# Kernel tuning notes

Measured on AMD Instinct MI355X. Metric: run time of the kernel, lower is better.

Reference implementation:

```python
import jax, jax.numpy as jnp
import numpy as np

N, E, R, D = 100000, 300000, 2, 128


def setup_inputs() -> dict:
    key = jax.random.key(0)
    k0, k1, k2, k3, k4 = jax.random.split(key, 5)
    x = jax.random.normal(k0, (N, D), dtype=jnp.float32)
    attn_w = jax.random.normal(k1, (R, 2 * D), dtype=jnp.float32) / np.sqrt(2 * D).astype(np.float32)
    loop_weight = jax.random.normal(k2, (D, D), dtype=jnp.float32) / np.sqrt(D).astype(np.float32)
    h_bias = jnp.zeros((D,), dtype=jnp.float32)
    src = jax.random.randint(k3, (R, E), 0, N, dtype=jnp.int32)
    dst = jax.random.randint(k4, (R, E), 0, N, dtype=jnp.int32)
    return {"x": x, "attn_w": attn_w, "loop_weight": loop_weight, "h_bias": h_bias,
            "src": src, "dst": dst}


def _rel_attention(x, a, src_r, dst_r):
    # Per-edge score: attn_fc(cat(src feat, dst feat)) with Linear(2D -> 1, no bias).
    d = x.shape[1]
    xs = x[src_r]                     # [E, D] gathered source features (the messages m)
    e = xs @ a[:d] + x[dst_r] @ a[d:]  # [E] edge logits (note: no leaky_relu in message_fc path)
    # Segment (per-destination mailbox) softmax, numerically stable.
    m = jax.ops.segment_max(e, dst_r, num_segments=N)
    p = jnp.exp(e - m[dst_r])
    denom = jax.ops.segment_sum(p, dst_r, num_segments=N)
    alpha = p / jnp.maximum(denom[dst_r], jnp.float32(1e-30))  # [E]
    # Weighted scatter-sum of messages back to destination nodes.
    return jax.ops.segment_sum(alpha[:, None] * xs, dst_r, num_segments=N)  # [N, D]


def reference(x, attn_w, loop_weight, h_bias, src, dst):
    # multi_update_all(..., 'sum'): sum the per-relation attention aggregations.
    agg = _rel_attention(x, attn_w[0], src[0], dst[0])
    for r in range(1, R):
        agg = agg + _rel_attention(x, attn_w[r], src[r], dst[r])
    # self loop + bias (activation=None, dropout=0)
    h = agg + x @ loop_weight + h_bias
    return h
```

## Files before the change

kernel.cpp:

```cpp
#include <hip/hip_runtime.h>

#define N_NODES 100000
#define N_EDGES 300000
#define DIM     128
#define NBINS   (2 * N_NODES)
#define CNT_STRIDE 8
#define SLOT_CAP 24
#define WCONV_BLOCKS 8
#define BIN_BLOCKS  ((N_EDGES + 255) / 256)
#define SCORE_BLOCKS (N_NODES / 4)
#define ZERO_BLOCKS ((NBINS * CNT_STRIDE / 4 + 255) / 256)
#define FUSE_BLOCKS (N_NODES / 16)

typedef __attribute__((ext_vector_type(8))) short bfrag;
typedef __attribute__((ext_vector_type(4))) float f32x4;

__device__ __forceinline__ unsigned short f2bf(float f) {
  unsigned int u = __float_as_uint(f);
  u += 0x7FFFu + ((u >> 16) & 1u);
  return (unsigned short)(u >> 16);
}
__device__ __forceinline__ float bflo(unsigned int u) { return __uint_as_float(u << 16); }
__device__ __forceinline__ float bfhi(unsigned int u) { return __uint_as_float(u & 0xffff0000u); }

__global__ __launch_bounds__(256) void k0_zero_kernel(int* __restrict__ counts) {
  int i = blockIdx.x * 256 + threadIdx.x;
  if (i < NBINS * CNT_STRIDE / 4) ((int4*)counts)[i] = make_int4(0, 0, 0, 0);
}

__global__ __launch_bounds__(256) void k1_bin_scores_kernel(
    const float* __restrict__ x, const float* __restrict__ attn_w,
    const float* __restrict__ W,
    const int* __restrict__ src, const int* __restrict__ dst,
    float* __restrict__ pexp, int* __restrict__ counts, int* __restrict__ slots,
    unsigned short* __restrict__ Wt, unsigned short* __restrict__ x_bf) {
  if (blockIdx.x < WCONV_BLOCKS) {
    for (int e = blockIdx.x * 256 + threadIdx.x; e < DIM * DIM; e += WCONV_BLOCKS * 256) {
      int k = e >> 7, c = e & 127;
      Wt[c * DIM + k] = f2bf(W[e]);
    }
    return;
  }
  if (blockIdx.x < WCONV_BLOCKS + BIN_BLOCKS) {
    int idx = (blockIdx.x - WCONV_BLOCKS) * 256 + threadIdx.x;
    if (idx < N_EDGES) {
      int d0 = dst[idx];
      int d1 = dst[idx + N_EDGES];
      int s0 = src[idx];
      int s1 = src[idx + N_EDGES];
      int p0 = atomicAdd(&counts[(size_t)(d0 * 2 + 0) * CNT_STRIDE], 1);
      int p1 = atomicAdd(&counts[(size_t)(d1 * 2 + 1) * CNT_STRIDE], 1);
      if (p0 < SLOT_CAP)
        __builtin_nontemporal_store(s0, &slots[(size_t)(d0 * 2 + 0) * SLOT_CAP + p0]);
      if (p1 < SLOT_CAP)
        __builtin_nontemporal_store(s1, &slots[(size_t)(d1 * 2 + 1) * SLOT_CAP + p1]);
    }
    return;
  }
  int wave = (((blockIdx.x - WCONV_BLOCKS - BIN_BLOCKS) * 256) + threadIdx.x) >> 6;
  int lane = threadIdx.x & 63;
  if (wave >= N_NODES) return;
  float2 a0 = ((const float2*)(attn_w +   0))[lane];
  float2 a1 = ((const float2*)(attn_w + 256))[lane];
  float2 v = ((const float2*)(x + (size_t)wave * DIM))[lane];
  ushort2 bv; bv.x = f2bf(v.x); bv.y = f2bf(v.y);
  ((ushort2*)(x_bf + (size_t)wave * DIM))[lane] = bv;
  float p0 = v.x * a0.x + v.y * a0.y;
  float p1 = v.x * a1.x + v.y * a1.y;
  #pragma unroll
  for (int off = 32; off > 0; off >>= 1) {
    p0 += __shfl_down(p0, off, 64);
    p1 += __shfl_down(p1, off, 64);
  }
  if (lane == 0) {
    pexp[wave]           = __expf(p0);
    pexp[N_NODES + wave] = __expf(p1);
  }
}

__global__ __launch_bounds__(256) void k2_gemm_agg_kernel(
    const int* __restrict__ slots, const int* __restrict__ counts,
    const float* __restrict__ pexp,
    const unsigned short* __restrict__ x_bf, const unsigned short* __restrict__ Wt,
    const float* __restrict__ bias, float* __restrict__ out) {
  __shared__ float gtile[16][DIM];
  int r0 = blockIdx.x * 16;
  int w  = threadIdx.x >> 6;
  int wl = threadIdx.x & 63;
  {
    int n = wl & 15, q = wl >> 4;
    const unsigned short* xrow = x_bf + (size_t)(r0 + n) * DIM;
    f32x4 acc[2];
    #pragma unroll
    for (int c = 0; c < 2; c++) {
      float bv = bias[(2 * w + c) * 16 + n];
      acc[c] = (f32x4){bv, bv, bv, bv};
    }
    #pragma unroll
    for (int kc = 0; kc < 4; kc++) {
      int k0 = kc * 32 + q * 8;
      bfrag a = *((const bfrag*)(xrow + k0));
      #pragma unroll
      for (int c = 0; c < 2; c++) {
        bfrag b = *((const bfrag*)(Wt + (size_t)((2 * w + c) * 16 + n) * DIM + k0));
        acc[c] = __builtin_amdgcn_mfma_f32_16x16x32_bf16(a, b, acc[c], 0, 0, 0);
      }
    }
    #pragma unroll
    for (int c = 0; c < 2; c++) {
      #pragma unroll
      for (int rr = 0; rr < 4; rr++) {
        gtile[q * 4 + rr][(2 * w + c) * 16 + n] = acc[c][rr];
      }
    }
  }
  __syncthreads();
  int rrel = wl >> 5;
  int l    = wl & 31;
  int nbase = r0 + w * 4;
  int cnt[4]; int sj[4]; float pj[4]; float dinv[4];
  #pragma unroll
  for (int nn = 0; nn < 4; nn++) {
    int c = counts[(size_t)((nbase + nn) * 2 + rrel) * CNT_STRIDE];
    cnt[nn] = (c > SLOT_CAP) ? SLOT_CAP : c;
  }
  #pragma unroll
  for (int nn = 0; nn < 4; nn++) {
    sj[nn] = 0;
    if (l < cnt[nn]) sj[nn] = slots[(size_t)((nbase + nn) * 2 + rrel) * SLOT_CAP + l];
  }
  #pragma unroll
  for (int nn = 0; nn < 4; nn++) {
    pj[nn] = (l < cnt[nn]) ? pexp[rrel * N_NODES + sj[nn]] : 0.f;
  }
  #pragma unroll
  for (int nn = 0; nn < 4; nn++) {
    float d = pj[nn];
    #pragma unroll
    for (int off = 16; off > 0; off >>= 1) d += __shfl_xor(d, off, 64);
    dinv[nn] = (cnt[nn] > 0) ? 1.f / d : 0.f;
  }
  #pragma unroll
  for (int nn = 0; nn < 4; nn++) {
    int node = nbase + nn;
    float4 accr = make_float4(0.f, 0.f, 0.f, 0.f);
    int cn = cnt[nn];
    int j = 0;
    for (; j + 4 <= cn; j += 4) {
      int   s0 = __shfl(sj[nn], j + 0, 32); float q0 = __shfl(pj[nn], j + 0, 32);
      int   s1 = __shfl(sj[nn], j + 1, 32); float q1 = __shfl(pj[nn], j + 1, 32);
      int   s2 = __shfl(sj[nn], j + 2, 32); float q2 = __shfl(pj[nn], j + 2, 32);
      int   s3 = __shfl(sj[nn], j + 3, 32); float q3 = __shfl(pj[nn], j + 3, 32);
      uint2 g0 = ((const uint2*)(x_bf + (size_t)s0 * DIM))[l];
      uint2 g1 = ((const uint2*)(x_bf + (size_t)s1 * DIM))[l];
      uint2 g2 = ((const uint2*)(x_bf + (size_t)s2 * DIM))[l];
      uint2 g3 = ((const uint2*)(x_bf + (size_t)s3 * DIM))[l];
      accr.x += q0*bflo(g0.x) + q1*bflo(g1.x) + q2*bflo(g2.x) + q3*bflo(g3.x);
      accr.y += q0*bfhi(g0.x) + q1*bfhi(g1.x) + q2*bfhi(g2.x) + q3*bfhi(g3.x);
      accr.z += q0*bflo(g0.y) + q1*bflo(g1.y) + q2*bflo(g2.y) + q3*bflo(g3.y);
      accr.w += q0*bfhi(g0.y) + q1*bfhi(g1.y) + q2*bfhi(g2.y) + q3*bfhi(g3.y);
    }
    for (; j < cn; j++) {
      int   s0 = __shfl(sj[nn], j, 32); float q0 = __shfl(pj[nn], j, 32);
      uint2 g0 = ((const uint2*)(x_bf + (size_t)s0 * DIM))[l];
      accr.x += q0*bflo(g0.x); accr.y += q0*bfhi(g0.x);
      accr.z += q0*bflo(g0.y); accr.w += q0*bfhi(g0.y);
    }
    float4 agg;
    agg.x = accr.x * dinv[nn];
    agg.y = accr.y * dinv[nn];
    agg.z = accr.z * dinv[nn];
    agg.w = accr.w * dinv[nn];
    agg.x += __shfl_xor(agg.x, 32, 64);
    agg.y += __shfl_xor(agg.y, 32, 64);
    agg.z += __shfl_xor(agg.z, 32, 64);
    agg.w += __shfl_xor(agg.w, 32, 64);
    if (wl < 32) {
      const float4 g = *((const float4*)&gtile[w * 4 + nn][4 * wl]);
      float4 o;
      o.x = g.x + agg.x;
      o.y = g.y + agg.y;
      o.z = g.z + agg.z;
      o.w = g.w + agg.w;
      ((float4*)(out + (size_t)node * DIM))[wl] = o;
    }
  }
}

extern "C" void kernel_launch(void* const* d_in, const int* in_sizes, int n_in,
                              void* d_out, int out_size, void* d_ws, size_t ws_size,
                              hipStream_t stream) {
  const float* x      = (const float*)d_in[0];
  const float* attn_w = (const float*)d_in[1];
  const float* loop_w = (const float*)d_in[2];
  const float* h_bias = (const float*)d_in[3];
  const int*   src    = (const int*)d_in[4];
  const int*   dst    = (const int*)d_in[5];
  float*       out    = (float*)d_out;

  float*          pexp   = (float*)d_ws;
  int*            counts = (int*)(pexp + NBINS);
  int*            slots  = counts + (size_t)NBINS * CNT_STRIDE;
  unsigned short* Wt     = (unsigned short*)(slots + (size_t)NBINS * SLOT_CAP);
  unsigned short* x_bf   = Wt + DIM * DIM;

  k0_zero_kernel<<<ZERO_BLOCKS, 256, 0, stream>>>(counts);
  k1_bin_scores_kernel<<<WCONV_BLOCKS + BIN_BLOCKS + SCORE_BLOCKS, 256, 0, stream>>>(
      x, attn_w, loop_w, src, dst, pexp, counts, slots, Wt, x_bf);
  k2_gemm_agg_kernel<<<FUSE_BLOCKS, 256, 0, stream>>>(
      slots, counts, pexp, x_bf, Wt, h_bias, out);
}
```

Baseline: 227.7 us.

## Merge three kernels into one persistent cooperative kernel with grid syncs

Replaces the zero/bin/score/GEMM-aggregate kernel sequence with a single cooperative persistent kernel that uses grid-wide syncs between phases. The bf16 transposed weight is built straight into swizzled LDS per block instead of global memory. Scores are now computed 16 lanes per row, and the neighbor gather is unrolled so up to six row loads per node are issued up front. The aim is to remove launch gaps and boost memory-level parallelism, at the cost of two grid barriers, lower occupancy from the 32KB LDS, and a fallback three-kernel path when cooperative launch is unavailable.

```diff
diff --git a/kernel.cpp b/kernel.cpp
--- a/kernel.cpp
+++ b/kernel.cpp
@@ -1,4 +1,7 @@
 #include <hip/hip_runtime.h>
+#include <hip/hip_cooperative_groups.h>
+
+namespace cg = cooperative_groups;
 
 #define N_NODES 100000
 #define N_EDGES 300000
@@ -6,14 +9,13 @@
 #define NBINS   (2 * N_NODES)
 #define CNT_STRIDE 8
 #define SLOT_CAP 24
-#define WCONV_BLOCKS 8
-#define BIN_BLOCKS  ((N_EDGES + 255) / 256)
-#define SCORE_BLOCKS (N_NODES / 4)
-#define ZERO_BLOCKS ((NBINS * CNT_STRIDE / 4 + 255) / 256)
-#define FUSE_BLOCKS (N_NODES / 16)
+#define ROW_TILES (N_NODES / 16)
+#define UNR 6
 
 typedef __attribute__((ext_vector_type(8))) short bfrag;
 typedef __attribute__((ext_vector_type(4))) float f32x4;
+typedef __attribute__((ext_vector_type(4))) unsigned short u16x4;
+typedef __attribute__((ext_vector_type(2))) unsigned int   u32x2;
 
 __device__ __forceinline__ unsigned short f2bf(float f) {
   unsigned int u = __float_as_uint(f);
@@ -23,70 +25,82 @@
 __device__ __forceinline__ float bflo(unsigned int u) { return __uint_as_float(u << 16); }
 __device__ __forceinline__ float bfhi(unsigned int u) { return __uint_as_float(u & 0xffff0000u); }
 
-__global__ __launch_bounds__(256) void k0_zero_kernel(int* __restrict__ counts) {
-  int i = blockIdx.x * 256 + threadIdx.x;
-  if (i < NBINS * CNT_STRIDE / 4) ((int4*)counts)[i] = make_int4(0, 0, 0, 0);
-}
-
-__global__ __launch_bounds__(256) void k1_bin_scores_kernel(
-    const float* __restrict__ x, const float* __restrict__ attn_w,
-    const float* __restrict__ W,
-    const int* __restrict__ src, const int* __restrict__ dst,
-    float* __restrict__ pexp, int* __restrict__ counts, int* __restrict__ slots,
-    unsigned short* __restrict__ Wt, unsigned short* __restrict__ x_bf) {
-  if (blockIdx.x < WCONV_BLOCKS) {
-    for (int e = blockIdx.x * 256 + threadIdx.x; e < DIM * DIM; e += WCONV_BLOCKS * 256) {
-      int k = e >> 7, c = e & 127;
-      Wt[c * DIM + k] = f2bf(W[e]);
-    }
-    return;
-  }
-  if (blockIdx.x < WCONV_BLOCKS + BIN_BLOCKS) {
-    int idx = (blockIdx.x - WCONV_BLOCKS) * 256 + threadIdx.x;
-    if (idx < N_EDGES) {
-      int d0 = dst[idx];
-      int d1 = dst[idx + N_EDGES];
-      int s0 = src[idx];
-      int s1 = src[idx + N_EDGES];
-      int p0 = atomicAdd(&counts[(size_t)(d0 * 2 + 0) * CNT_STRIDE], 1);
-      int p1 = atomicAdd(&counts[(size_t)(d1 * 2 + 1) * CNT_STRIDE], 1);
-      if (p0 < SLOT_CAP)
-        __builtin_nontemporal_store(s0, &slots[(size_t)(d0 * 2 + 0) * SLOT_CAP + p0]);
-      if (p1 < SLOT_CAP)
-        __builtin_nontemporal_store(s1, &slots[(size_t)(d1 * 2 + 1) * SLOT_CAP + p1]);
-    }
-    return;
-  }
-  int wave = (((blockIdx.x - WCONV_BLOCKS - BIN_BLOCKS) * 256) + threadIdx.x) >> 6;
-  int lane = threadIdx.x & 63;
-  if (wave >= N_NODES) return;
-  float2 a0 = ((const float2*)(attn_w +   0))[lane];
-  float2 a1 = ((const float2*)(attn_w + 256))[lane];
-  float2 v = ((const float2*)(x + (size_t)wave * DIM))[lane];
-  ushort2 bv; bv.x = f2bf(v.x); bv.y = f2bf(v.y);
-  ((ushort2*)(x_bf + (size_t)wave * DIM))[lane] = bv;
-  float p0 = v.x * a0.x + v.y * a0.y;
-  float p1 = v.x * a1.x + v.y * a1.y;
-  #pragma unroll
-  for (int off = 32; off > 0; off >>= 1) {
-    p0 += __shfl_down(p0, off, 64);
-    p1 += __shfl_down(p1, off, 64);
-  }
-  if (lane == 0) {
-    pexp[wave]           = __expf(p0);
-    pexp[N_NODES + wave] = __expf(p1);
-  }
-}
-
-__global__ __launch_bounds__(256) void k2_gemm_agg_kernel(
+__device__ __forceinline__ void do_zero(int* counts, int start, int stride) {
+  for (int i = start; i < NBINS * CNT_STRIDE / 4; i += stride)
+    ((int4*)counts)[i] = make_int4(0, 0, 0, 0);
+}
+
+__device__ __forceinline__ void do_wt_lds(unsigned short* WtS, const float* W, int tid) {
+  for (int e = tid; e < DIM * DIM; e += 256) {
+    int k = e >> 7, c = e & 127;
+    int byte = c * 256 + k * 2;
+    int swz = byte ^ ((c & 7) << 4);
+    WtS[swz >> 1] = f2bf(W[e]);
+  }
+}
+
+__device__ __forceinline__ void do_bin(const int* __restrict__ src,
+                                       const int* __restrict__ dst,
+                                       int* __restrict__ counts, int* __restrict__ slots,
+                                       int start, int stride) {
+  for (int e = start; e < N_EDGES; e += stride) {
+    int d0 = __builtin_nontemporal_load(&dst[e]);
+    int d1 = __builtin_nontemporal_load(&dst[e + N_EDGES]);
+    int s0 = __builtin_nontemporal_load(&src[e]);
+    int s1 = __builtin_nontemporal_load(&src[e + N_EDGES]);
+    int p0 = atomicAdd(&counts[(size_t)(d0 * 2 + 0) * CNT_STRIDE], 1);
+    int p1 = atomicAdd(&counts[(size_t)(d1 * 2 + 1) * CNT_STRIDE], 1);
+    if (p0 < SLOT_CAP)
+      __builtin_nontemporal_store(s0, &slots[(size_t)(d0 * 2 + 0) * SLOT_CAP + p0]);
+    if (p1 < SLOT_CAP)
+      __builtin_nontemporal_store(s1, &slots[(size_t)(d1 * 2 + 1) * SLOT_CAP + p1]);
+  }
+}
+
+__device__ __forceinline__ void do_scores(const float* __restrict__ x,
+                                          const float* __restrict__ attn_w,
+                                          float* __restrict__ pexp,
+                                          unsigned short* __restrict__ x_bf,
+                                          int tid, int bstart, int bstride) {
+  int t    = tid & 15;
+  int rsub = tid >> 4;
+  const f32x4* A0 = (const f32x4*)attn_w;
+  const f32x4* A1 = (const f32x4*)(attn_w + 2 * DIM);
+  f32x4 a00 = A0[t], a01 = A0[t + 16];
+  f32x4 a10 = A1[t], a11 = A1[t + 16];
+  for (int tb = bstart; tb < ROW_TILES; tb += bstride) {
+    int row = tb * 16 + rsub;
+    const f32x4* xr = (const f32x4*)(x + (size_t)row * DIM);
+    f32x4 v0 = __builtin_nontemporal_load(xr + t);
+    f32x4 v1 = __builtin_nontemporal_load(xr + t + 16);
+    u16x4 b0, b1;
+    b0.x = f2bf(v0.x); b0.y = f2bf(v0.y); b0.z = f2bf(v0.z); b0.w = f2bf(v0.w);
+    b1.x = f2bf(v1.x); b1.y = f2bf(v1.y); b1.z = f2bf(v1.z); b1.w = f2bf(v1.w);
+    u16x4* xb = (u16x4*)(x_bf + (size_t)row * DIM);
+    xb[t] = b0; xb[t + 16] = b1;
+    float p0 = v0.x*a00.x + v0.y*a00.y + v0.z*a00.z + v0.w*a00.w
+             + v1.x*a01.x + v1.y*a01.y + v1.z*a01.z + v1.w*a01.w;
+    float p1 = v0.x*a10.x + v0.y*a10.y + v0.z*a10.z + v0.w*a10.w
+             + v1.x*a11.x + v1.y*a11.y + v1.z*a11.z + v1.w*a11.w;
+    #pragma unroll
+    for (int off = 8; off > 0; off >>= 1) {
+      p0 += __shfl_xor(p0, off, 64);
+      p1 += __shfl_xor(p1, off, 64);
+    }
+    if (t == 0) {
+      pexp[row]           = __expf(p0);
+      pexp[N_NODES + row] = __expf(p1);
+    }
+  }
+}
+
+__device__ __forceinline__ void do_tile(const unsigned short* WtS, float (*gtile)[DIM],
     const int* __restrict__ slots, const int* __restrict__ counts,
-    const float* __restrict__ pexp,
-    const unsigned short* __restrict__ x_bf, const unsigned short* __restrict__ Wt,
-    const float* __restrict__ bias, float* __restrict__ out) {
-  __shared__ float gtile[16][DIM];
-  int r0 = blockIdx.x * 16;
-  int w  = threadIdx.x >> 6;
-  int wl = threadIdx.x & 63;
+    const float* __restrict__ pexp, const unsigned short* __restrict__ x_bf,
+    const float* __restrict__ bias, float* __restrict__ out, int tid, int tb) {
+  int r0 = tb * 16;
+  int w  = tid >> 6;
+  int wl = tid & 63;
   {
     int n = wl & 15, q = wl >> 4;
     const unsigned short* xrow = x_bf + (size_t)(r0 + n) * DIM;
@@ -102,21 +116,21 @@
       bfrag a = *((const bfrag*)(xrow + k0));
       #pragma unroll
       for (int c = 0; c < 2; c++) {
-        bfrag b = *((const bfrag*)(Wt + (size_t)((2 * w + c) * 16 + n) * DIM + k0));
-        acc[c] = __builtin_amdgcn_mfma_f32_16x16x32_bf16(a, b, acc[c], 0, 0, 0);
+        int cc   = (2 * w + c) * 16 + n;
+        int byte = cc * 256 + k0 * 2;
+        const bfrag* bp = (const bfrag*)((const char*)WtS + (byte ^ ((cc & 7) << 4)));
+        acc[c] = __builtin_amdgcn_mfma_f32_16x16x32_bf16(a, *bp, acc[c], 0, 0, 0);
       }
     }
     #pragma unroll
-    for (int c = 0; c < 2; c++) {
+    for (int c = 0; c < 2; c++)
       #pragma unroll
-      for (int rr = 0; rr < 4; rr++) {
+      for (int rr = 0; rr < 4; rr++)
         gtile[q * 4 + rr][(2 * w + c) * 16 + n] = acc[c][rr];
-      }
-    }
   }
   __syncthreads();
-  int rrel = wl >> 5;
-  int l    = wl & 31;
+  int rrel  = wl >> 5;
+  int l     = wl & 31;
   int nbase = r0 + w * 4;
   int cnt[4]; int sj[4]; float pj[4]; float dinv[4];
   #pragma unroll
@@ -125,14 +139,11 @@
     cnt[nn] = (c > SLOT_CAP) ? SLOT_CAP : c;
   }
   #pragma unroll
-  for (int nn = 0; nn < 4; nn++) {
-    sj[nn] = 0;
-    if (l < cnt[nn]) sj[nn] = slots[(size_t)((nbase + nn) * 2 + rrel) * SLOT_CAP + l];
-  }
-  #pragma unroll
-  for (int nn = 0; nn < 4; nn++) {
+  for (int nn = 0; nn < 4; nn++)
+    sj[nn] = (l < cnt[nn]) ? slots[(size_t)((nbase + nn) * 2 + rrel) * SLOT_CAP + l] : 0;
+  #pragma unroll
+  for (int nn = 0; nn < 4; nn++)
     pj[nn] = (l < cnt[nn]) ? pexp[rrel * N_NODES + sj[nn]] : 0.f;
-  }
   #pragma unroll
   for (int nn = 0; nn < 4; nn++) {
     float d = pj[nn];
@@ -140,51 +151,112 @@
     for (int off = 16; off > 0; off >>= 1) d += __shfl_xor(d, off, 64);
     dinv[nn] = (cnt[nn] > 0) ? 1.f / d : 0.f;
   }
-  #pragma unroll
-  for (int nn = 0; nn < 4; nn++) {
-    int node = nbase + nn;
-    float4 accr = make_float4(0.f, 0.f, 0.f, 0.f);
-    int cn = cnt[nn];
-    int j = 0;
-    for (; j + 4 <= cn; j += 4) {
-      int   s0 = __shfl(sj[nn], j + 0, 32); float q0 = __shfl(pj[nn], j + 0, 32);
-      int   s1 = __shfl(sj[nn], j + 1, 32); float q1 = __shfl(pj[nn], j + 1, 32);
-      int   s2 = __shfl(sj[nn], j + 2, 32); float q2 = __shfl(pj[nn], j + 2, 32);
-      int   s3 = __shfl(sj[nn], j + 3, 32); float q3 = __shfl(pj[nn], j + 3, 32);
-      uint2 g0 = ((const uint2*)(x_bf + (size_t)s0 * DIM))[l];
-      uint2 g1 = ((const uint2*)(x_bf + (size_t)s1 * DIM))[l];
-      uint2 g2 = ((const uint2*)(x_bf + (size_t)s2 * DIM))[l];
-      uint2 g3 = ((const uint2*)(x_bf + (size_t)s3 * DIM))[l];
-      accr.x += q0*bflo(g0.x) + q1*bflo(g1.x) + q2*bflo(g2.x) + q3*bflo(g3.x);
-      accr.y += q0*bfhi(g0.x) + q1*bfhi(g1.x) + q2*bfhi(g2.x) + q3*bfhi(g3.x);
-      accr.z += q0*bflo(g0.y) + q1*bflo(g1.y) + q2*bflo(g2.y) + q3*bflo(g3.y);
-      accr.w += q0*bfhi(g0.y) + q1*bfhi(g1.y) + q2*bfhi(g2.y) + q3*bfhi(g3.y);
-    }
-    for (; j < cn; j++) {
-      int   s0 = __shfl(sj[nn], j, 32); float q0 = __shfl(pj[nn], j, 32);
-      uint2 g0 = ((const uint2*)(x_bf + (size_t)s0 * DIM))[l];
-      accr.x += q0*bflo(g0.x); accr.y += q0*bfhi(g0.x);
-      accr.z += q0*bflo(g0.y); accr.w += q0*bfhi(g0.y);
-    }
-    float4 agg;
-    agg.x = accr.x * dinv[nn];
-    agg.y = accr.y * dinv[nn];
-    agg.z = accr.z * dinv[nn];
-    agg.w = accr.w * dinv[nn];
+  u32x2 g[4][UNR];
+  #pragma unroll
+  for (int nn = 0; nn < 4; nn++) {
+    #pragma unroll
+    for (int u = 0; u < UNR; u++) {
+      int s = __shfl(sj[nn], u, 32);
+      if (u < cnt[nn])
+        g[nn][u] = ((const u32x2*)(x_bf + (size_t)s * DIM))[l];
+    }
+  }
+  f32x4 accr[4];
+  #pragma unroll
+  for (int nn = 0; nn < 4; nn++) accr[nn] = (f32x4){0.f, 0.f, 0.f, 0.f};
+  #pragma unroll
+  for (int nn = 0; nn < 4; nn++) {
+    #pragma unroll
+    for (int u = 0; u < UNR; u++) {
+      float qv = __shfl(pj[nn], u, 32);
+      if (u < cnt[nn]) {
+        u32x2 gv = g[nn][u];
+        accr[nn].x += qv * bflo(gv.x);
+        accr[nn].y += qv * bfhi(gv.x);
+        accr[nn].z += qv * bflo(gv.y);
+        accr[nn].w += qv * bfhi(gv.y);
+      }
+    }
+  }
+  #pragma unroll
+  for (int nn = 0; nn < 4; nn++) {
+    for (int j = UNR; j < cnt[nn]; j++) {
+      int   s  = __shfl(sj[nn], j, 32);
+      float qv = __shfl(pj[nn], j, 32);
+      u32x2 gv = ((const u32x2*)(x_bf + (size_t)s * DIM))[l];
+      accr[nn].x += qv * bflo(gv.x); accr[nn].y += qv * bfhi(gv.x);
+      accr[nn].z += qv * bflo(gv.y); accr[nn].w += qv * bfhi(gv.y);
+    }
+  }
+  #pragma unroll
+  for (int nn = 0; nn < 4; nn++) {
+    f32x4 agg;
+    agg.x = accr[nn].x * dinv[nn];
+    agg.y = accr[nn].y * dinv[nn];
+    agg.z = accr[nn].z * dinv[nn];
+    agg.w = accr[nn].w * dinv[nn];
     agg.x += __shfl_xor(agg.x, 32, 64);
     agg.y += __shfl_xor(agg.y, 32, 64);
     agg.z += __shfl_xor(agg.z, 32, 64);
     agg.w += __shfl_xor(agg.w, 32, 64);
     if (wl < 32) {
-      const float4 g = *((const float4*)&gtile[w * 4 + nn][4 * wl]);
-      float4 o;
-      o.x = g.x + agg.x;
-      o.y = g.y + agg.y;
-      o.z = g.z + agg.z;
-      o.w = g.w + agg.w;
-      ((float4*)(out + (size_t)node * DIM))[wl] = o;
-    }
-  }
+      const float* gr = &gtile[w * 4 + nn][4 * wl];
+      f32x4 o;
+      o.x = gr[0] + agg.x; o.y = gr[1] + agg.y;
+      o.z = gr[2] + agg.z; o.w = gr[3] + agg.w;
+      __builtin_nontemporal_store(o, (f32x4*)(out + (size_t)(nbase + nn) * DIM) + wl);
+    }
+  }
+  __syncthreads();
+}
+
+__global__ __launch_bounds__(256, 4) void mega_kernel(
+    const float* __restrict__ x, const float* __restrict__ attn_w,
+    const float* __restrict__ W, const float* __restrict__ bias,
+    const int* __restrict__ src, const int* __restrict__ dst,
+    float* __restrict__ pexp, int* __restrict__ counts, int* __restrict__ slots,
+    unsigned short* __restrict__ x_bf, float* __restrict__ out) {
+  __shared__ unsigned short WtS[DIM * DIM];
+  __shared__ float gtile[16][DIM];
+  int tid  = threadIdx.x;
+  int gtid = blockIdx.x * 256 + tid;
+  int gsz  = gridDim.x * 256;
+  do_wt_lds(WtS, W, tid);
+  do_zero(counts, gtid, gsz);
+  cg::this_grid().sync();
+  do_bin(src, dst, counts, slots, gtid, gsz);
+  do_scores(x, attn_w, pexp, x_bf, tid, blockIdx.x, gridDim.x);
+  cg::this_grid().sync();
+  for (int tb = blockIdx.x; tb < ROW_TILES; tb += gridDim.x)
+    do_tile(WtS, gtile, slots, counts, pexp, x_bf, bias, out, tid, tb);
+}
+
+#define FB_BIN_BLOCKS ((N_EDGES + 255) / 256)
+
+__global__ __launch_bounds__(256) void fb_k0(int* __restrict__ counts) {
+  do_zero(counts, blockIdx.x * 256 + threadIdx.x, gridDim.x * 256);
+}
+__global__ __launch_bounds__(256) void fb_k1(
+    const float* __restrict__ x, const float* __restrict__ attn_w,
+    const int* __restrict__ src, const int* __restrict__ dst,
+    float* __restrict__ pexp, int* __restrict__ counts, int* __restrict__ slots,
+    unsigned short* __restrict__ x_bf) {
+  if (blockIdx.x < FB_BIN_BLOCKS) {
+    do_bin(src, dst, counts, slots, blockIdx.x * 256 + threadIdx.x, FB_BIN_BLOCKS * 256);
+    return;
+  }
+  do_scores(x, attn_w, pexp, x_bf, threadIdx.x, blockIdx.x - FB_BIN_BLOCKS, ROW_TILES);
+}
+__global__ __launch_bounds__(256) void fb_k2(
+    const float* __restrict__ W, const int* __restrict__ slots,
+    const int* __restrict__ counts, const float* __restrict__ pexp,
+    const unsigned short* __restrict__ x_bf, const float* __restrict__ bias,
+    float* __restrict__ out) {
+  __shared__ unsigned short WtS[DIM * DIM];
+  __shared__ float gtile[16][DIM];
+  do_wt_lds(WtS, W, threadIdx.x);
+  __syncthreads();
+  do_tile(WtS, gtile, slots, counts, pexp, x_bf, bias, out, threadIdx.x, blockIdx.x);
 }
 
 extern "C" void kernel_launch(void* const* d_in, const int* in_sizes, int n_in,
@@ -201,12 +273,26 @@
   float*          pexp   = (float*)d_ws;
   int*            counts = (int*)(pexp + NBINS);
   int*            slots  = counts + (size_t)NBINS * CNT_STRIDE;
-  unsigned short* Wt     = (unsigned short*)(slots + (size_t)NBINS * SLOT_CAP);
-  unsigned short* x_bf   = Wt + DIM * DIM;
-
-  k0_zero_kernel<<<ZERO_BLOCKS, 256, 0, stream>>>(counts);
-  k1_bin_scores_kernel<<<WCONV_BLOCKS + BIN_BLOCKS + SCORE_BLOCKS, 256, 0, stream>>>(
-      x, attn_w, loop_w, src, dst, pexp, counts, slots, Wt, x_bf);
-  k2_gemm_agg_kernel<<<FUSE_BLOCKS, 256, 0, stream>>>(
-      slots, counts, pexp, x_bf, Wt, h_bias, out);
-}
+  unsigned short* x_bf   = (unsigned short*)(slots + (size_t)NBINS * SLOT_CAP);
+
+  static int coop_blocks = -2;
+  if (coop_blocks == -2) {
+    int bpc = 0;
+    hipError_t qe = hipOccupancyMaxActiveBlocksPerMultiprocessor(
+        &bpc, (const void*)mega_kernel, 256, 0);
+    coop_blocks = (qe == hipSuccess && bpc >= 1) ? bpc * 256 : -1;
+  }
+  if (coop_blocks > 0) {
+    void* args[] = {(void*)&x, (void*)&attn_w, (void*)&loop_w, (void*)&h_bias,
+                    (void*)&src, (void*)&dst, (void*)&pexp, (void*)&counts,
+                    (void*)&slots, (void*)&x_bf, (void*)&out};
+    hipError_t le = hipLaunchCooperativeKernel((const void*)mega_kernel,
+        dim3(coop_blocks), dim3(256), args, 0, stream);
+    if (le == hipSuccess) return;
+    coop_blocks = -1;
+  }
+  fb_k0<<<(NBINS * CNT_STRIDE / 4 + 255) / 256, 256, 0, stream>>>(counts);
+  fb_k1<<<FB_BIN_BLOCKS + ROW_TILES, 256, 0, stream>>>(
+      x, attn_w, src, dst, pexp, counts, slots, x_bf);
+  fb_k2<<<ROW_TILES, 256, 0, stream>>>(loop_w, slots, counts, pexp, x_bf, h_bias, out);
+}
```

Result: slower. 484.3 us (+112.7%).

## Batch first four neighbor gathers across nodes and use nontemporal memory ops

Applied to the files above, without the earlier changes.

The aggregation kernel now issues the first four neighbor-row gathers for all four nodes of a wave up front, masked by zero weights. Before, it walked each node's edges one node at a time. This raises memory-level parallelism for the typical low-degree mailboxes, at the cost of extra loads for nodes with fewer than four edges. It also loads slot indices unconditionally and pads the shared-memory tile. Edge, feature and output traffic now uses nontemporal loads and stores, and the count-zeroing kernel is replaced with hipMemsetAsync.

```diff
diff --git a/kernel.cpp b/kernel.cpp
--- a/kernel.cpp
+++ b/kernel.cpp
@@ -6,14 +6,17 @@
 #define NBINS   (2 * N_NODES)
 #define CNT_STRIDE 8
 #define SLOT_CAP 24
+#define ROW_TILES (N_NODES / 16)
+#define GDIM (DIM + 4)
+
 #define WCONV_BLOCKS 8
 #define BIN_BLOCKS  ((N_EDGES + 255) / 256)
 #define SCORE_BLOCKS (N_NODES / 4)
-#define ZERO_BLOCKS ((NBINS * CNT_STRIDE / 4 + 255) / 256)
-#define FUSE_BLOCKS (N_NODES / 16)
 
 typedef __attribute__((ext_vector_type(8))) short bfrag;
 typedef __attribute__((ext_vector_type(4))) float f32x4;
+typedef __attribute__((ext_vector_type(2))) float f32x2;
+typedef __attribute__((ext_vector_type(2))) unsigned int   u32x2;
 
 __device__ __forceinline__ unsigned short f2bf(float f) {
   unsigned int u = __float_as_uint(f);
@@ -23,12 +26,7 @@
 __device__ __forceinline__ float bflo(unsigned int u) { return __uint_as_float(u << 16); }
 __device__ __forceinline__ float bfhi(unsigned int u) { return __uint_as_float(u & 0xffff0000u); }
 
-__global__ __launch_bounds__(256) void k0_zero_kernel(int* __restrict__ counts) {
-  int i = blockIdx.x * 256 + threadIdx.x;
-  if (i < NBINS * CNT_STRIDE / 4) ((int4*)counts)[i] = make_int4(0, 0, 0, 0);
-}
-
-__global__ __launch_bounds__(256) void k1_bin_scores_kernel(
+__global__ __launch_bounds__(256) void k1_kernel(
     const float* __restrict__ x, const float* __restrict__ attn_w,
     const float* __restrict__ W,
     const int* __restrict__ src, const int* __restrict__ dst,
@@ -42,12 +40,12 @@
     return;
   }
   if (blockIdx.x < WCONV_BLOCKS + BIN_BLOCKS) {
-    int idx = (blockIdx.x - WCONV_BLOCKS) * 256 + threadIdx.x;
-    if (idx < N_EDGES) {
-      int d0 = dst[idx];
-      int d1 = dst[idx + N_EDGES];
-      int s0 = src[idx];
-      int s1 = src[idx + N_EDGES];
+    int e = (blockIdx.x - WCONV_BLOCKS) * 256 + threadIdx.x;
+    if (e < N_EDGES) {
+      int d0 = __builtin_nontemporal_load(&dst[e]);
+      int d1 = __builtin_nontemporal_load(&dst[e + N_EDGES]);
+      int s0 = __builtin_nontemporal_load(&src[e]);
+      int s1 = __builtin_nontemporal_load(&src[e + N_EDGES]);
       int p0 = atomicAdd(&counts[(size_t)(d0 * 2 + 0) * CNT_STRIDE], 1);
       int p1 = atomicAdd(&counts[(size_t)(d1 * 2 + 1) * CNT_STRIDE], 1);
       if (p0 < SLOT_CAP)
@@ -57,12 +55,12 @@
     }
     return;
   }
-  int wave = (((blockIdx.x - WCONV_BLOCKS - BIN_BLOCKS) * 256) + threadIdx.x) >> 6;
+  int wave = (((blockIdx.x - WCONV_BLOCKS - BIN_BLOCKS) * 256) + (int)threadIdx.x) >> 6;
   int lane = threadIdx.x & 63;
   if (wave >= N_NODES) return;
-  float2 a0 = ((const float2*)(attn_w +   0))[lane];
-  float2 a1 = ((const float2*)(attn_w + 256))[lane];
-  float2 v = ((const float2*)(x + (size_t)wave * DIM))[lane];
+  f32x2 a0 = ((const f32x2*)(attn_w +   0))[lane];
+  f32x2 a1 = ((const f32x2*)(attn_w + 256))[lane];
+  f32x2 v = __builtin_nontemporal_load(((const f32x2*)(x + (size_t)wave * DIM)) + lane);
   ushort2 bv; bv.x = f2bf(v.x); bv.y = f2bf(v.y);
   ((ushort2*)(x_bf + (size_t)wave * DIM))[lane] = bv;
   float p0 = v.x * a0.x + v.y * a0.y;
@@ -78,15 +76,16 @@
   }
 }
 
-__global__ __launch_bounds__(256) void k2_gemm_agg_kernel(
+__global__ __launch_bounds__(256) void k2_kernel(
     const int* __restrict__ slots, const int* __restrict__ counts,
-    const float* __restrict__ pexp,
-    const unsigned short* __restrict__ x_bf, const unsigned short* __restrict__ Wt,
-    const float* __restrict__ bias, float* __restrict__ out) {
-  __shared__ float gtile[16][DIM];
-  int r0 = blockIdx.x * 16;
-  int w  = threadIdx.x >> 6;
-  int wl = threadIdx.x & 63;
+    const float* __restrict__ pexp, const unsigned short* __restrict__ x_bf,
+    const unsigned short* __restrict__ Wt, const float* __restrict__ bias,
+    float* __restrict__ out) {
+  __shared__ float gtile[16][GDIM];
+  int tid = threadIdx.x;
+  int r0  = blockIdx.x * 16;
+  int w   = tid >> 6;
+  int wl  = tid & 63;
   {
     int n = wl & 15, q = wl >> 4;
     const unsigned short* xrow = x_bf + (size_t)(r0 + n) * DIM;
@@ -107,82 +106,107 @@
       }
     }
     #pragma unroll
-    for (int c = 0; c < 2; c++) {
+    for (int c = 0; c < 2; c++)
       #pragma unroll
-      for (int rr = 0; rr < 4; rr++) {
+      for (int rr = 0; rr < 4; rr++)
         gtile[q * 4 + rr][(2 * w + c) * 16 + n] = acc[c][rr];
-      }
-    }
   }
   __syncthreads();
-  int rrel = wl >> 5;
-  int l    = wl & 31;
+  int rrel  = wl >> 5;
+  int l     = wl & 31;
   int nbase = r0 + w * 4;
-  int cnt[4]; int sj[4]; float pj[4]; float dinv[4];
-  #pragma unroll
-  for (int nn = 0; nn < 4; nn++) {
-    int c = counts[(size_t)((nbase + nn) * 2 + rrel) * CNT_STRIDE];
-    cnt[nn] = (c > SLOT_CAP) ? SLOT_CAP : c;
-  }
-  #pragma unroll
-  for (int nn = 0; nn < 4; nn++) {
-    sj[nn] = 0;
-    if (l < cnt[nn]) sj[nn] = slots[(size_t)((nbase + nn) * 2 + rrel) * SLOT_CAP + l];
-  }
-  #pragma unroll
-  for (int nn = 0; nn < 4; nn++) {
-    pj[nn] = (l < cnt[nn]) ? pexp[rrel * N_NODES + sj[nn]] : 0.f;
-  }
-  #pragma unroll
-  for (int nn = 0; nn < 4; nn++) {
+  int craw[4], sraw[4];
+  #pragma unroll
+  for (int nn = 0; nn < 4; nn++)
+    craw[nn] = counts[(size_t)((nbase + nn) * 2 + rrel) * CNT_STRIDE];
+  #pragma unroll
+  for (int nn = 0; nn < 4; nn++)
+    sraw[nn] = slots[(size_t)((nbase + nn) * 2 + rrel) * SLOT_CAP + l];
+  int cnt[4]; int sj[4];
+  #pragma unroll
+  for (int nn = 0; nn < 4; nn++) {
+    cnt[nn] = (craw[nn] > SLOT_CAP) ? SLOT_CAP : craw[nn];
+    sj[nn]  = (l < cnt[nn]) ? sraw[nn] : 0;
+  }
+  float pl[4];
+  #pragma unroll
+  for (int nn = 0; nn < 4; nn++)
+    pl[nn] = pexp[rrel * N_NODES + sj[nn]];
+  float pj[4]; float dinv[4];
+  #pragma unroll
+  for (int nn = 0; nn < 4; nn++) {
+    pj[nn] = (l < cnt[nn]) ? pl[nn] : 0.f;
     float d = pj[nn];
     #pragma unroll
     for (int off = 16; off > 0; off >>= 1) d += __shfl_xor(d, off, 64);
     dinv[nn] = (cnt[nn] > 0) ? 1.f / d : 0.f;
   }
-  #pragma unroll
-  for (int nn = 0; nn < 4; nn++) {
-    int node = nbase + nn;
-    float4 accr = make_float4(0.f, 0.f, 0.f, 0.f);
+  u32x2 g[4][4];
+  #pragma unroll
+  for (int u = 0; u < 4; u++) {
+    #pragma unroll
+    for (int nn = 0; nn < 4; nn++) {
+      int s = __shfl(sj[nn], u, 32);
+      g[nn][u] = ((const u32x2*)(x_bf + (size_t)s * DIM))[l];
+    }
+  }
+  f32x4 accr[4];
+  #pragma unroll
+  for (int nn = 0; nn < 4; nn++) accr[nn] = (f32x4){0.f, 0.f, 0.f, 0.f};
+  #pragma unroll
+  for (int nn = 0; nn < 4; nn++) {
+    #pragma unroll
+    for (int u = 0; u < 4; u++) {
+      float qv = __shfl(pj[nn], u, 32);
+      u32x2 gv = g[nn][u];
+      accr[nn].x += qv * bflo(gv.x);
+      accr[nn].y += qv * bfhi(gv.x);
+      accr[nn].z += qv * bflo(gv.y);
+      accr[nn].w += qv * bfhi(gv.y);
+    }
+  }
+  #pragma unroll
+  for (int nn = 0; nn < 4; nn++) {
     int cn = cnt[nn];
-    int j = 0;
+    int j = 4;
     for (; j + 4 <= cn; j += 4) {
       int   s0 = __shfl(sj[nn], j + 0, 32); float q0 = __shfl(pj[nn], j + 0, 32);
       int   s1 = __shfl(sj[nn], j + 1, 32); float q1 = __shfl(pj[nn], j + 1, 32);
       int   s2 = __shfl(sj[nn], j + 2, 32); float q2 = __shfl(pj[nn], j + 2, 32);
       int   s3 = __shfl(sj[nn], j + 3, 32); float q3 = __shfl(pj[nn], j + 3, 32);
-      uint2 g0 = ((const uint2*)(x_bf + (size_t)s0 * DIM))[l];
-      uint2 g1 = ((const uint2*)(x_bf + (size_t)s1 * DIM))[l];
-      uint2 g2 = ((const uint2*)(x_bf + (size_t)s2 * DIM))[l];
-      uint2 g3 = ((const uint2*)(x_bf + (size_t)s3 * DIM))[l];
-      accr.x += q0*bflo(g0.x) + q1*bflo(g1.x) + q2*bflo(g2.x) + q3*bflo(g3.x);
-      accr.y += q0*bfhi(g0.x) + q1*bfhi(g1.x) + q2*bfhi(g2.x) + q3*bfhi(g3.x);
-      accr.z += q0*bflo(g0.y) + q1*bflo(g1.y) + q2*bflo(g2.y) + q3*bflo(g3.y);
-      accr.w += q0*bfhi(g0.y) + q1*bfhi(g1.y) + q2*bfhi(g2.y) + q3*bfhi(g3.y);
+      u32x2 g0 = ((const u32x2*)(x_bf + (size_t)s0 * DIM))[l];
+      u32x2 g1 = ((const u32x2*)(x_bf + (size_t)s1 * DIM))[l];
+      u32x2 g2 = ((const u32x2*)(x_bf + (size_t)s2 * DIM))[l];
+      u32x2 g3 = ((const u32x2*)(x_bf + (size_t)s3 * DIM))[l];
+      accr[nn].x += q0*bflo(g0.x) + q1*bflo(g1.x) + q2*bflo(g2.x) + q3*bflo(g3.x);
+      accr[nn].y += q0*bfhi(g0.x) + q1*bfhi(g1.x) + q2*bfhi(g2.x) + q3*bfhi(g3.x);
+      accr[nn].z += q0*bflo(g0.y) + q1*bflo(g1.y) + q2*bflo(g2.y) + q3*bflo(g3.y);
+      accr[nn].w += q0*bfhi(g0.y) + q1*bfhi(g1.y) + q2*bfhi(g2.y) + q3*bfhi(g3.y);
     }
     for (; j < cn; j++) {
       int   s0 = __shfl(sj[nn], j, 32); float q0 = __shfl(pj[nn], j, 32);
-      uint2 g0 = ((const uint2*)(x_bf + (size_t)s0 * DIM))[l];
-      accr.x += q0*bflo(g0.x); accr.y += q0*bfhi(g0.x);
-      accr.z += q0*bflo(g0.y); accr.w += q0*bfhi(g0.y);
-    }
-    float4 agg;
-    agg.x = accr.x * dinv[nn];
-    agg.y = accr.y * dinv[nn];
-    agg.z = accr.z * dinv[nn];
-    agg.w = accr.w * dinv[nn];
+      u32x2 g0 = ((const u32x2*)(x_bf + (size_t)s0 * DIM))[l];
+      accr[nn].x += q0*bflo(g0.x); accr[nn].y += q0*bfhi(g0.x);
+      accr[nn].z += q0*bflo(g0.y); accr[nn].w += q0*bfhi(g0.y);
+    }
+  }
+  #pragma unroll
+  for (int nn = 0; nn < 4; nn++) {
+    f32x4 agg;
+    agg.x = accr[nn].x * dinv[nn];
+    agg.y = accr[nn].y * dinv[nn];
+    agg.z = accr[nn].z * dinv[nn];
+    agg.w = accr[nn].w * dinv[nn];
     agg.x += __shfl_xor(agg.x, 32, 64);
     agg.y += __shfl_xor(agg.y, 32, 64);
     agg.z += __shfl_xor(agg.z, 32, 64);
     agg.w += __shfl_xor(agg.w, 32, 64);
     if (wl < 32) {
-      const float4 g = *((const float4*)&gtile[w * 4 + nn][4 * wl]);
-      float4 o;
-      o.x = g.x + agg.x;
-      o.y = g.y + agg.y;
-      o.z = g.z + agg.z;
-      o.w = g.w + agg.w;
-      ((float4*)(out + (size_t)node * DIM))[wl] = o;
+      const float* gr = &gtile[w * 4 + nn][4 * wl];
+      f32x4 o;
+      o.x = gr[0] + agg.x; o.y = gr[1] + agg.y;
+      o.z = gr[2] + agg.z; o.w = gr[3] + agg.w;
+      __builtin_nontemporal_store(o, (f32x4*)(out + (size_t)(r0 + w * 4 + nn) * DIM) + wl);
     }
   }
 }
@@ -204,9 +228,9 @@
   unsigned short* Wt     = (unsigned short*)(slots + (size_t)NBINS * SLOT_CAP);
   unsigned short* x_bf   = Wt + DIM * DIM;
 
-  k0_zero_kernel<<<ZERO_BLOCKS, 256, 0, stream>>>(counts);
-  k1_bin_scores_kernel<<<WCONV_BLOCKS + BIN_BLOCKS + SCORE_BLOCKS, 256, 0, stream>>>(
+  hipMemsetAsync(counts, 0, (size_t)NBINS * CNT_STRIDE * sizeof(int), stream);
+  k1_kernel<<<WCONV_BLOCKS + BIN_BLOCKS + SCORE_BLOCKS, 256, 0, stream>>>(
       x, attn_w, loop_w, src, dst, pexp, counts, slots, Wt, x_bf);
-  k2_gemm_agg_kernel<<<FUSE_BLOCKS, 256, 0, stream>>>(
+  k2_kernel<<<ROW_TILES, 256, 0, stream>>>(
       slots, counts, pexp, x_bf, Wt, h_bias, out);
 }
```

Result: faster. 221.7 us (-2.6%).
